# Kernel tuning notes

Measured on AMD Instinct MI355X. Metric: run time of the kernel, lower is better.

## Reference

```python
import jax, jax.numpy as jnp
import numpy as np

N_NODES = 100000
N_EDGES = 1250000
N_PAIRS = 200000
IN_DIM = 128
HID = 64
N_LAYERS = 3


def setup_inputs() -> dict:
    key = jax.random.key(0)
    ks = jax.random.split(key, 16)
    x = jax.random.normal(ks[0], (N_NODES, IN_DIM), dtype=jnp.float32)
    edge_index = jax.random.randint(ks[1], (2, N_EDGES), 0, N_NODES, dtype=jnp.int64)
    pair_index = jax.random.randint(ks[2], (N_PAIRS, 2), 0, N_NODES, dtype=jnp.int64)
    s_in = 1.0 / np.sqrt(IN_DIM)
    s_h = 1.0 / np.sqrt(HID)
    s_2h = 1.0 / np.sqrt(2 * HID)
    enc_W = jax.random.uniform(ks[3], (IN_DIM, HID), jnp.float32, -s_in, s_in)
    enc_b = jax.random.uniform(ks[4], (HID,), jnp.float32, -s_in, s_in)
    # SAGEConv params per layer: lin_l (neighbors, with bias), lin_r (root, no bias)
    Wl = jax.random.uniform(ks[5], (N_LAYERS, HID, HID), jnp.float32, -s_h, s_h)
    bl = jax.random.uniform(ks[6], (N_LAYERS, HID), jnp.float32, -s_h, s_h)
    Wr = jax.random.uniform(ks[7], (N_LAYERS, HID, HID), jnp.float32, -s_h, s_h)
    # predictor MLP: Linear(2h -> h), ReLU, Linear(h -> 1)
    W1 = jax.random.uniform(ks[8], (2 * HID, HID), jnp.float32, -s_2h, s_2h)
    b1 = jax.random.uniform(ks[9], (HID,), jnp.float32, -s_2h, s_2h)
    W2 = jax.random.uniform(ks[10], (HID, 1), jnp.float32, -s_h, s_h)
    b2 = jax.random.uniform(ks[11], (1,), jnp.float32, -s_h, s_h)
    return {"x": x, "edge_index": edge_index, "pair_index": pair_index,
            "enc_W": enc_W, "enc_b": enc_b, "Wl": Wl, "bl": bl, "Wr": Wr,
            "W1": W1, "b1": b1, "W2": W2, "b2": b2}


def reference(x, edge_index, pair_index, enc_W, enc_b, Wl, bl, Wr, W1, b1, W2, b2):
    src, dst = edge_index[0], edge_index[1]
    n = x.shape[0]
    # neighbor counts for mean aggregation (empty neighborhoods -> 0, matching PyG)
    deg = jax.ops.segment_sum(jnp.ones((src.shape[0],), x.dtype), dst, num_segments=n)
    inv_deg = jnp.where(deg > 0, 1.0 / jnp.maximum(deg, 1.0), 0.0)[:, None]  # [N,1]
    # node encoder: Linear + ReLU
    h = jax.nn.relu(x @ enc_W + enc_b)  # [N, HID]
    for i in range(Wl.shape[0]):
        # scatter-mean of source features onto destinations
        agg = jax.ops.segment_sum(h[src], dst, num_segments=n) * inv_deg  # [N, HID]
        h = jax.nn.relu(agg @ Wl[i] + bl[i] + h @ Wr[i])
        # dropout is identity in eval mode
    z = jnp.concatenate([h[pair_index[:, 0]], h[pair_index[:, 1]]], axis=1)  # [P, 2*HID]
    out = (jax.nn.relu(z @ W1 + b1) @ W2 + b2)[:, 0]  # [P]
    return out
```

## Files before the change

### kernel.cpp

```cpp
#include <hip/hip_runtime.h>
#include <hip/hip_fp16.h>
#include <cstdint>
#include <cstddef>

#define N_NODES_C 100000
#define N_EDGES_C 1250000
#define N_PAIRS_C 200000
#define IN_DIM_C 128
#define HID_C 64

#define NB_S 256
#define BSH 9
#define NPB 512
#define NBKT 196
#define SEG_CAP 8192

typedef _Float16 f16x8 __attribute__((ext_vector_type(8)));
typedef float f32x4 __attribute__((ext_vector_type(4)));


#define SCAN_TPB 256
#define SCAN_IPT 4
#define SCAN_ELEMS 1024

__global__ void k_scan_partial(const int* __restrict__ in, int* __restrict__ outp,
                               int* __restrict__ blocksums, int n) {
    __shared__ int sd[SCAN_TPB];
    int tid = threadIdx.x;
    int base = blockIdx.x * SCAN_ELEMS + tid * SCAN_IPT;
    int v[SCAN_IPT]; int s = 0;
    for (int k = 0; k < SCAN_IPT; k++) { int idx = base + k; v[k] = (idx < n) ? in[idx] : 0; s += v[k]; }
    sd[tid] = s;
    __syncthreads();
    for (int off = 1; off < SCAN_TPB; off <<= 1) {
        int t = (tid >= off) ? sd[tid - off] : 0;
        __syncthreads();
        sd[tid] += t;
        __syncthreads();
    }
    int excl = sd[tid] - s;
    for (int k = 0; k < SCAN_IPT; k++) { int idx = base + k; if (idx < n) outp[idx] = excl; excl += v[k]; }
    if (tid == SCAN_TPB - 1) blocksums[blockIdx.x] = sd[tid];
}

__global__ void k_scan_blocks(int* __restrict__ bs, int nb) {
    __shared__ int sd[128];
    int t = threadIdx.x;
    int v = (t < nb) ? bs[t] : 0;
    sd[t] = v;
    __syncthreads();
    for (int off = 1; off < 128; off <<= 1) {
        int u = (t >= off) ? sd[t - off] : 0;
        __syncthreads();
        sd[t] += u;
        __syncthreads();
    }
    if (t < nb) bs[t] = sd[t] - v;
}

__global__ void k_scan_addg(int* __restrict__ arr, const int* __restrict__ bs, int n) {
    int i = blockIdx.x * blockDim.x + threadIdx.x;
    if (i < n) arr[i] += bs[i >> 10];
}


__global__ __launch_bounds__(256) void k_hist(const int* __restrict__ dst,
                                              int* __restrict__ histT, int e) {
    __shared__ int lh[NBKT];
    int tid = threadIdx.x, k = blockIdx.x;
    if (tid < NBKT) lh[tid] = 0;
    __syncthreads();
    int chunk = (e + NB_S - 1) / NB_S;
    int i0 = k * chunk, i1 = min(i0 + chunk, e);
    for (int i = i0 + tid; i < i1; i += 256) atomicAdd(&lh[dst[i] >> BSH], 1);
    __syncthreads();
    if (tid < NBKT) histT[tid * NB_S + k] = lh[tid];
}

__global__ __launch_bounds__(256) void k_scatter(const int* __restrict__ edges,
                                                 const int* __restrict__ offs,
                                                 int2* __restrict__ staging, int e) {
    __shared__ int cur[NBKT];
    int tid = threadIdx.x, k = blockIdx.x;
    if (tid < NBKT) cur[tid] = offs[tid * NB_S + k];
    __syncthreads();
    int chunk = (e + NB_S - 1) / NB_S;
    int i0 = k * chunk, i1 = min(i0 + chunk, e);
    for (int i = i0 + tid; i < i1; i += 256) {
        int s = edges[i];
        int d = edges[e + i];
        int p = atomicAdd(&cur[d >> BSH], 1);
        staging[p] = make_int2(s, d);
    }
}

__global__ __launch_bounds__(256) void k_bucket_fill(const int2* __restrict__ staging,
        const int* __restrict__ offs, int* __restrict__ rowptr,
        float* __restrict__ invd, int* __restrict__ adj, int n, int e) {
    __shared__ int ldeg[NPB];
    __shared__ int lrow[NPB];
    __shared__ int ps[256];
    __shared__ int lseg[SEG_CAP];
    int tid = threadIdx.x, b = blockIdx.x;
    int n0 = b << BSH;
    int nn = min(NPB, n - n0);
    int segBeg = offs[b * NB_S];
    int segEnd = (b == NBKT - 1) ? e : offs[(b + 1) * NB_S];

    ldeg[tid] = 0; ldeg[tid + 256] = 0;
    __syncthreads();
    for (int i = segBeg + tid; i < segEnd; i += 256)
        atomicAdd(&ldeg[staging[i].y - n0], 1);
    __syncthreads();

    int a0 = ldeg[2 * tid], a1 = ldeg[2 * tid + 1];
    int s = a0 + a1;
    ps[tid] = s;
    __syncthreads();
    for (int off = 1; off < 256; off <<= 1) {
        int t = (tid >= off) ? ps[tid - off] : 0;
        __syncthreads();
        ps[tid] += t;
        __syncthreads();
    }
    int excl = ps[tid] - s;
    lrow[2 * tid] = excl;
    lrow[2 * tid + 1] = excl + a0;
    __syncthreads();

    for (int j = tid; j < nn; j += 256) {
        rowptr[n0 + j] = segBeg + lrow[j];
        int d = ldeg[j];
        invd[n0 + j] = (d > 0) ? (1.0f / (float)d) : 0.0f;
    }
    if (b == NBKT - 1 && tid == 0) rowptr[n] = e;
    __syncthreads();

    for (int i = segBeg + tid; i < segEnd; i += 256) {
        int2 ed = staging[i];
        int p = atomicAdd(&lrow[ed.y - n0], 1);
        if (p < SEG_CAP) lseg[p] = ed.x;
        else adj[segBeg + p] = ed.x;
    }
    __syncthreads();

    int m = segEnd - segBeg; if (m > SEG_CAP) m = SEG_CAP;
    for (int p = tid; p < m; p += 256) adj[segBeg + p] = lseg[p];
}


__global__ __launch_bounds__(256) void k_aggregate(const int* __restrict__ rowptr,
        const int* __restrict__ adj, const float* __restrict__ invd,
        const __half* __restrict__ hin16, __half* __restrict__ agg16, int n) {
    int wid = threadIdx.x >> 6, lane = threadIdx.x & 63;
    int nodeA = (blockIdx.x * 4 + wid) * 2;
    if (nodeA >= n) return;
    const int half_ = lane >> 5;
    const int c2 = (lane & 31) * 2;
    int node = nodeA + half_;
    bool valid = node < n;
    int nodec = valid ? node : n - 1;
    int beg = rowptr[nodec], end = rowptr[nodec + 1];
    float accx = 0.f, accy = 0.f;
    for (int e = beg; e < end; e += 8) {
        int idx[8];
        #pragma unroll
        for (int j = 0; j < 8; ++j) {
            int ee = e + j;
            idx[j] = adj[ee < end ? ee : end - 1];
        }
        __half2 v[8];
        #pragma unroll
        for (int j = 0; j < 8; ++j)
            v[j] = *(const __half2*)&hin16[(size_t)idx[j] * HID_C + c2];
        #pragma unroll
        for (int j = 0; j < 8; ++j) {
            float2 f = __half22float2(v[j]);
            bool in = (e + j < end);
            accx += in ? f.x : 0.f;
            accy += in ? f.y : 0.f;
        }
    }
    if (valid) {
        float s = invd[node];
        *(__half2*)&agg16[(size_t)node * HID_C + c2] =
            __floats2half2_rn(accx * s, accy * s);
    }
}


__device__ __forceinline__ float4 ld4(const float* p) { return *(const float4*)p; }


template<int SRC>
__global__ __launch_bounds__(256, 2) void k_mm(
    const float* __restrict__ A1f,
    const __half* __restrict__ A1h, const __half* __restrict__ A2h,
    const float* __restrict__ Ws1, const float* __restrict__ Ws2,
    const float* __restrict__ bias,
    float* __restrict__ outp, __half* __restrict__ out16, int nrows)
{
    __shared__ __half Ah[128 * 128];
    __shared__ __half Bt[64 * 128];
    const int t = threadIdx.x;
    const int g0 = blockIdx.x * 128;

    #pragma unroll
    for (int p = 0; p < 8; ++p) {
        int li = p * 256 + t;
        int r = li >> 4;
        int o = li & 15;
        int g = g0 + r; if (g > nrows - 1) g = nrows - 1;
        f16x8 v;
        if (SRC == 0) {
            const float* src = A1f + (size_t)g * 128 + o * 8;
            float4 f0 = ld4(src), f1 = ld4(src + 4);
            v[0] = (_Float16)f0.x; v[1] = (_Float16)f0.y;
            v[2] = (_Float16)f0.z; v[3] = (_Float16)f0.w;
            v[4] = (_Float16)f1.x; v[5] = (_Float16)f1.y;
            v[6] = (_Float16)f1.z; v[7] = (_Float16)f1.w;
        } else {
            const __half* src = (o < 8) ? (A1h + (size_t)g * 64 + o * 8)
                                        : (A2h + (size_t)g * 64 + (o - 8) * 8);
            v = *(const f16x8*)src;
        }
        *(f16x8*)&Ah[r * 128 + (o ^ (r & 15)) * 8] = v;
    }
    #pragma unroll
    for (int p = 0; p < 32; ++p) {
        int li = p * 256 + t;
        int c = li & 63;
        int k = li >> 6;
        float wv;
        if (SRC == 0) wv = Ws1[k * 64 + c];
        else          wv = (k < 64) ? Ws1[k * 64 + c] : Ws2[(k - 64) * 64 + c];
        Bt[c * 128 + (((k >> 3) ^ (c & 15)) * 8) + (k & 7)] = __float2half(wv);
    }
    __syncthreads();

    const int lane = t & 63;
    const int wid = t >> 6;
    const int R = wid * 32;
    const int lr = lane & 15;
    const int lk = lane >> 4;

    f32x4 acc[2][4];
    #pragma unroll
    for (int fr = 0; fr < 2; ++fr)
        #pragma unroll
        for (int fc = 0; fc < 4; ++fc)
            acc[fr][fc] = (f32x4){0.f, 0.f, 0.f, 0.f};

    #pragma unroll
    for (int ks = 0; ks < 4; ++ks) {
        int o = ks * 4 + lk;
        f16x8 af0, af1;
        {
            int r0 = R + lr;
            int r1 = R + 16 + lr;
            af0 = *(const f16x8*)&Ah[r0 * 128 + (o ^ (r0 & 15)) * 8];
            af1 = *(const f16x8*)&Ah[r1 * 128 + (o ^ (r1 & 15)) * 8];
        }
        #pragma unroll
        for (int fc = 0; fc < 4; ++fc) {
            int c = fc * 16 + lr;
            f16x8 bf = *(const f16x8*)&Bt[c * 128 + (o ^ (c & 15)) * 8];
            acc[0][fc] = __builtin_amdgcn_mfma_f32_16x16x32_f16(af0, bf, acc[0][fc], 0, 0, 0);
            acc[1][fc] = __builtin_amdgcn_mfma_f32_16x16x32_f16(af1, bf, acc[1][fc], 0, 0, 0);
        }
    }

    float bv[4];
    #pragma unroll
    for (int fc = 0; fc < 4; ++fc) bv[fc] = bias[fc * 16 + lr];
    #pragma unroll
    for (int fr = 0; fr < 2; ++fr) {
        #pragma unroll
        for (int j = 0; j < 4; ++j) {
            int gr = g0 + R + fr * 16 + lk * 4 + j;
            if (gr < nrows) {
                #pragma unroll
                for (int fc = 0; fc < 4; ++fc) {
                    int col = fc * 16 + lr;
                    float v = fmaxf(acc[fr][fc][j] + bv[fc], 0.f);
                    outp[(size_t)gr * 64 + col] = v;
                    if (out16) out16[(size_t)gr * 64 + col] = __float2half(v);
                }
            }
        }
    }
}


__global__ __launch_bounds__(256, 2) void k_uvm(
    const float* __restrict__ H, const float* __restrict__ W1,
    float* __restrict__ U, float* __restrict__ V, int nrows)
{
    __shared__ __half Ah[128 * 64];
    __shared__ __half Bt[128 * 64];
    const int t = threadIdx.x;
    const int g0 = blockIdx.x * 128;

    #pragma unroll
    for (int p = 0; p < 4; ++p) {
        int li = p * 256 + t;
        int r = li >> 3;
        int o = li & 7;
        int g = g0 + r; if (g > nrows - 1) g = nrows - 1;
        const float* src = H + (size_t)g * 64 + o * 8;
        float4 f0 = ld4(src), f1 = ld4(src + 4);
        f16x8 v;
        v[0] = (_Float16)f0.x; v[1] = (_Float16)f0.y;
        v[2] = (_Float16)f0.z; v[3] = (_Float16)f0.w;
        v[4] = (_Float16)f1.x; v[5] = (_Float16)f1.y;
        v[6] = (_Float16)f1.z; v[7] = (_Float16)f1.w;
        *(f16x8*)&Ah[r * 64 + (o ^ (r & 7)) * 8] = v;
    }
    #pragma unroll
    for (int p = 0; p < 32; ++p) {
        int li = p * 256 + t;
        int c = li >> 6;
        int k = li & 63;
        float wv = (c < 64) ? W1[k * 64 + c] : W1[(64 + k) * 64 + (c - 64)];
        Bt[c * 64 + (((k >> 3) ^ (c & 7)) * 8) + (k & 7)] = __float2half(wv);
    }
    __syncthreads();

    const int lane = t & 63;
    const int wid = t >> 6;
    const int R = wid * 32;
    const int lr = lane & 15;
    const int lk = lane >> 4;

    f32x4 acc[2][8];
    #pragma unroll
    for (int fr = 0; fr < 2; ++fr)
        #pragma unroll
        for (int fc = 0; fc < 8; ++fc)
            acc[fr][fc] = (f32x4){0.f, 0.f, 0.f, 0.f};

    #pragma unroll
    for (int ks = 0; ks < 2; ++ks) {
        int o = ks * 4 + lk;
        int r0 = R + lr, r1 = R + 16 + lr;
        f16x8 af0 = *(const f16x8*)&Ah[r0 * 64 + (o ^ (r0 & 7)) * 8];
        f16x8 af1 = *(const f16x8*)&Ah[r1 * 64 + (o ^ (r1 & 7)) * 8];
        #pragma unroll
        for (int fc = 0; fc < 8; ++fc) {
            int c = fc * 16 + lr;
            f16x8 bf = *(const f16x8*)&Bt[c * 64 + (o ^ (c & 7)) * 8];
            acc[0][fc] = __builtin_amdgcn_mfma_f32_16x16x32_f16(af0, bf, acc[0][fc], 0, 0, 0);
            acc[1][fc] = __builtin_amdgcn_mfma_f32_16x16x32_f16(af1, bf, acc[1][fc], 0, 0, 0);
        }
    }

    #pragma unroll
    for (int fr = 0; fr < 2; ++fr) {
        #pragma unroll
        for (int j = 0; j < 4; ++j) {
            int gr = g0 + R + fr * 16 + lk * 4 + j;
            if (gr < nrows) {
                #pragma unroll
                for (int fc = 0; fc < 8; ++fc) {
                    int col = fc * 16 + lr;
                    float v = acc[fr][fc][j];
                    if (col < 64) U[(size_t)gr * 64 + col] = v;
                    else          V[(size_t)gr * 64 + (col - 64)] = v;
                }
            }
        }
    }
}

__global__ __launch_bounds__(256) void k_pred(
    const float* __restrict__ U, const float* __restrict__ V,
    const int* __restrict__ pidx, const float* __restrict__ b1,
    const float* __restrict__ W2, const float* __restrict__ b2,
    float* __restrict__ outp, int np)
{
    const int t = threadIdx.x;
    const int lg = t & 15;
    const int p = blockIdx.x * 16 + (t >> 4);
    float4 bv = ld4(b1 + lg * 4);
    float4 wv = ld4(W2 + lg * 4);
    if (p >= np) return;
    int2 ab = ((const int2*)pidx)[p];
    float4 u = ld4(U + (size_t)ab.x * 64 + lg * 4);
    float4 v = ld4(V + (size_t)ab.y * 64 + lg * 4);
    float zx = fmaxf(u.x + v.x + bv.x, 0.f);
    float zy = fmaxf(u.y + v.y + bv.y, 0.f);
    float zz = fmaxf(u.z + v.z + bv.z, 0.f);
    float zw = fmaxf(u.w + v.w + bv.w, 0.f);
    float s = zx * wv.x + zy * wv.y + zz * wv.z + zw * wv.w;
    s += __shfl_down(s, 8, 16);
    s += __shfl_down(s, 4, 16);
    s += __shfl_down(s, 2, 16);
    s += __shfl_down(s, 1, 16);
    if (lg == 0) outp[p] = s + b2[0];
}


extern "C" void kernel_launch(void* const* d_in, const int* in_sizes, int n_in,
                              void* d_out, int out_size, void* d_ws, size_t ws_size,
                              hipStream_t stream) {
    const float* x    = (const float*)d_in[0];
    const int*   edges= (const int*)d_in[1];
    const int*   pair = (const int*)d_in[2];
    const float* encW = (const float*)d_in[3];
    const float* encb = (const float*)d_in[4];
    const float* Wl   = (const float*)d_in[5];
    const float* bl   = (const float*)d_in[6];
    const float* Wr   = (const float*)d_in[7];
    const float* W1   = (const float*)d_in[8];
    const float* b1   = (const float*)d_in[9];
    const float* W2   = (const float*)d_in[10];
    const float* b2   = (const float*)d_in[11];
    float* out = (float*)d_out;

    const int N = N_NODES_C, E = N_EDGES_C, P = N_PAIRS_C;
    const int* dst = edges + E;
    const int M = NBKT * NB_S;

    char* w = (char*)d_ws;
    auto alloc = [&](size_t bytes) { char* p = w; w += (bytes + 255) & ~(size_t)255; return p; };
    int*   rowptr = (int*)alloc((size_t)(N + 1) * 4);
    int*   histT  = (int*)alloc((size_t)M * 4);
    int*   offs   = (int*)alloc((size_t)M * 4);
    int*   bsums  = (int*)alloc(128 * 4);
    float* invd   = (float*)alloc((size_t)N * 4);
    int*   adj    = (int*)alloc((size_t)E * 4);
    float* h0     = (float*)alloc((size_t)N * HID_C * 4);
    float* h1     = (float*)alloc((size_t)N * HID_C * 4);
    float* agg    = (float*)alloc((size_t)N * HID_C * 4);
    __half* h16a  = (__half*)alloc((size_t)N * HID_C * 2);
    __half* h16b  = (__half*)alloc((size_t)N * HID_C * 2);
    __half* agg16 = (__half*)alloc((size_t)N * HID_C * 2);
    int2*  staging= (int2*)agg;

    int nscan = (M + SCAN_ELEMS - 1) / SCAN_ELEMS;

    hipLaunchKernelGGL(k_hist, dim3(NB_S), dim3(256), 0, stream, dst, histT, E);
    hipLaunchKernelGGL(k_scan_partial, dim3(nscan), dim3(SCAN_TPB), 0, stream, histT, offs, bsums, M);
    hipLaunchKernelGGL(k_scan_blocks, dim3(1), dim3(128), 0, stream, bsums, nscan);
    hipLaunchKernelGGL(k_scan_addg, dim3((M + 255) / 256), dim3(256), 0, stream, offs, bsums, M);
    hipLaunchKernelGGL(k_scatter, dim3(NB_S), dim3(256), 0, stream, edges, offs, staging, E);
    hipLaunchKernelGGL(k_bucket_fill, dim3(NBKT), dim3(256), 0, stream, staging, offs, rowptr, invd, adj, N, E);

    const int NB128 = (N + 127) / 128;

    k_mm<0><<<dim3(NB128), dim3(256), 0, stream>>>(
        x, nullptr, nullptr, encW, nullptr, encb, h0, h16a, N);

    float* hc = h0; float* hn = h1;
    __half* h16c = h16a; __half* h16n = h16b;
    for (int l = 0; l < 3; l++) {
        hipLaunchKernelGGL(k_aggregate, dim3((N / 2 + 3) / 4), dim3(256), 0, stream,
                           rowptr, adj, invd, h16c, agg16, N);
        k_mm<1><<<dim3(NB128), dim3(256), 0, stream>>>(
            nullptr, agg16, h16c, Wl + (size_t)l * 64 * 64, Wr + (size_t)l * 64 * 64,
            bl + (size_t)l * 64, hn, (l < 2) ? h16n : (__half*)nullptr, N);
        float* tswap = hc; hc = hn; hn = tswap;
        __half* t16 = h16c; h16c = h16n; h16n = t16;
    }

    float* Ubuf = agg;
    float* Vbuf = hn;
    const int NB_UV = (N + 127) / 128;
    hipLaunchKernelGGL(k_uvm, dim3(NB_UV), dim3(256), 0, stream, hc, W1, Ubuf, Vbuf, N);
    hipLaunchKernelGGL(k_pred, dim3((P + 15) / 16), dim3(256), 0, stream,
                       Ubuf, Vbuf, pair, b1, W2, b2, out, P);
}
```

Before: 341.5 us.

## Widen aggregation to 4 nodes per wave and store U/V in fp16

The aggregate kernel now has each wave handle four nodes with 16 lanes per node, and each lane loads 8 bytes (four fp16 values) per neighbour instead of 4 bytes. The predictor intermediates U and V are written and gathered as fp16 instead of fp32, which halves the random-gather traffic in the pair predictor. The W1 staging loop is reindexed so consecutive threads read consecutive global columns. The cost is extra fp16 rounding in U and V, plus per-lane indirection overhead that is now spread across fewer lanes.

```diff
diff --git a/kernel.cpp b/kernel.cpp
--- a/kernel.cpp
+++ b/kernel.cpp
@@ -153,15 +153,15 @@
         const int* __restrict__ adj, const float* __restrict__ invd,
         const __half* __restrict__ hin16, __half* __restrict__ agg16, int n) {
     int wid = threadIdx.x >> 6, lane = threadIdx.x & 63;
-    int nodeA = (blockIdx.x * 4 + wid) * 2;
-    if (nodeA >= n) return;
-    const int half_ = lane >> 5;
-    const int c2 = (lane & 31) * 2;
-    int node = nodeA + half_;
+    int node0 = (blockIdx.x * 4 + wid) * 4;
+    if (node0 >= n) return;
+    const int q = lane >> 4;
+    const int c4 = (lane & 15) * 4;
+    int node = node0 + q;
     bool valid = node < n;
     int nodec = valid ? node : n - 1;
     int beg = rowptr[nodec], end = rowptr[nodec + 1];
-    float accx = 0.f, accy = 0.f;
+    float a0 = 0.f, a1 = 0.f, a2 = 0.f, a3 = 0.f;
     for (int e = beg; e < end; e += 8) {
         int idx[8];
         #pragma unroll
@@ -169,22 +169,29 @@
             int ee = e + j;
             idx[j] = adj[ee < end ? ee : end - 1];
         }
-        __half2 v[8];
+        float2 raw[8];
         #pragma unroll
         for (int j = 0; j < 8; ++j)
-            v[j] = *(const __half2*)&hin16[(size_t)idx[j] * HID_C + c2];
+            raw[j] = *(const float2*)&hin16[(size_t)idx[j] * HID_C + c4];
         #pragma unroll
         for (int j = 0; j < 8; ++j) {
-            float2 f = __half22float2(v[j]);
+            union { float f; __half2 h; } ulo, uhi;
+            ulo.f = raw[j].x; uhi.f = raw[j].y;
+            float2 f0 = __half22float2(ulo.h);
+            float2 f1 = __half22float2(uhi.h);
             bool in = (e + j < end);
-            accx += in ? f.x : 0.f;
-            accy += in ? f.y : 0.f;
+            a0 += in ? f0.x : 0.f;
+            a1 += in ? f0.y : 0.f;
+            a2 += in ? f1.x : 0.f;
+            a3 += in ? f1.y : 0.f;
         }
     }
     if (valid) {
         float s = invd[node];
-        *(__half2*)&agg16[(size_t)node * HID_C + c2] =
-            __floats2half2_rn(accx * s, accy * s);
+        union { float f; __half2 h; } s0, s1;
+        s0.h = __floats2half2_rn(a0 * s, a1 * s);
+        s1.h = __floats2half2_rn(a2 * s, a3 * s);
+        *(float2*)&agg16[(size_t)node * HID_C + c4] = make_float2(s0.f, s1.f);
     }
 }
 
@@ -294,7 +301,7 @@
 
 __global__ __launch_bounds__(256, 2) void k_uvm(
     const float* __restrict__ H, const float* __restrict__ W1,
-    float* __restrict__ U, float* __restrict__ V, int nrows)
+    __half* __restrict__ U16, __half* __restrict__ V16, int nrows)
 {
     __shared__ __half Ah[128 * 64];
     __shared__ __half Bt[128 * 64];
@@ -319,8 +326,8 @@
     #pragma unroll
     for (int p = 0; p < 32; ++p) {
         int li = p * 256 + t;
-        int c = li >> 6;
-        int k = li & 63;
+        int c = li & 127;
+        int k = li >> 7;
         float wv = (c < 64) ? W1[k * 64 + c] : W1[(64 + k) * 64 + (c - 64)];
         Bt[c * 64 + (((k >> 3) ^ (c & 7)) * 8) + (k & 7)] = __float2half(wv);
     }
@@ -363,9 +370,9 @@
                 #pragma unroll
                 for (int fc = 0; fc < 8; ++fc) {
                     int col = fc * 16 + lr;
-                    float v = acc[fr][fc][j];
-                    if (col < 64) U[(size_t)gr * 64 + col] = v;
-                    else          V[(size_t)gr * 64 + (col - 64)] = v;
+                    __half v = __float2half(acc[fr][fc][j]);
+                    if (col < 64) U16[(size_t)gr * 64 + col] = v;
+                    else          V16[(size_t)gr * 64 + (col - 64)] = v;
                 }
             }
         }
@@ -373,7 +380,7 @@
 }
 
 __global__ __launch_bounds__(256) void k_pred(
-    const float* __restrict__ U, const float* __restrict__ V,
+    const __half* __restrict__ U16, const __half* __restrict__ V16,
     const int* __restrict__ pidx, const float* __restrict__ b1,
     const float* __restrict__ W2, const float* __restrict__ b2,
     float* __restrict__ outp, int np)
@@ -385,12 +392,16 @@
     float4 wv = ld4(W2 + lg * 4);
     if (p >= np) return;
     int2 ab = ((const int2*)pidx)[p];
-    float4 u = ld4(U + (size_t)ab.x * 64 + lg * 4);
-    float4 v = ld4(V + (size_t)ab.y * 64 + lg * 4);
-    float zx = fmaxf(u.x + v.x + bv.x, 0.f);
-    float zy = fmaxf(u.y + v.y + bv.y, 0.f);
-    float zz = fmaxf(u.z + v.z + bv.z, 0.f);
-    float zw = fmaxf(u.w + v.w + bv.w, 0.f);
+    float2 ur = *(const float2*)&U16[(size_t)ab.x * 64 + lg * 4];
+    float2 vr = *(const float2*)&V16[(size_t)ab.y * 64 + lg * 4];
+    union { float f; __half2 h; } u0, u1, v0, v1;
+    u0.f = ur.x; u1.f = ur.y; v0.f = vr.x; v1.f = vr.y;
+    float2 ua = __half22float2(u0.h), ub = __half22float2(u1.h);
+    float2 va = __half22float2(v0.h), vb = __half22float2(v1.h);
+    float zx = fmaxf(ua.x + va.x + bv.x, 0.f);
+    float zy = fmaxf(ua.y + va.y + bv.y, 0.f);
+    float zz = fmaxf(ub.x + vb.x + bv.z, 0.f);
+    float zw = fmaxf(ub.y + vb.y + bv.w, 0.f);
     float s = zx * wv.x + zy * wv.y + zz * wv.z + zw * wv.w;
     s += __shfl_down(s, 8, 16);
     s += __shfl_down(s, 4, 16);
@@ -435,6 +446,8 @@
     __half* h16a  = (__half*)alloc((size_t)N * HID_C * 2);
     __half* h16b  = (__half*)alloc((size_t)N * HID_C * 2);
     __half* agg16 = (__half*)alloc((size_t)N * HID_C * 2);
+    __half* U16   = (__half*)alloc((size_t)N * HID_C * 2);
+    __half* V16   = (__half*)alloc((size_t)N * HID_C * 2);
     int2*  staging= (int2*)agg;
 
     int nscan = (M + SCAN_ELEMS - 1) / SCAN_ELEMS;
@@ -454,7 +467,7 @@
     float* hc = h0; float* hn = h1;
     __half* h16c = h16a; __half* h16n = h16b;
     for (int l = 0; l < 3; l++) {
-        hipLaunchKernelGGL(k_aggregate, dim3((N / 2 + 3) / 4), dim3(256), 0, stream,
+        hipLaunchKernelGGL(k_aggregate, dim3((N + 15) / 16), dim3(256), 0, stream,
                            rowptr, adj, invd, h16c, agg16, N);
         k_mm<1><<<dim3(NB128), dim3(256), 0, stream>>>(
             nullptr, agg16, h16c, Wl + (size_t)l * 64 * 64, Wr + (size_t)l * 64 * 64,
@@ -463,10 +476,8 @@
         __half* t16 = h16c; h16c = h16n; h16n = t16;
     }
 
-    float* Ubuf = agg;
-    float* Vbuf = hn;
     const int NB_UV = (N + 127) / 128;
-    hipLaunchKernelGGL(k_uvm, dim3(NB_UV), dim3(256), 0, stream, hc, W1, Ubuf, Vbuf, N);
+    hipLaunchKernelGGL(k_uvm, dim3(NB_UV), dim3(256), 0, stream, hc, W1, U16, V16, N);
     hipLaunchKernelGGL(k_pred, dim3((P + 15) / 16), dim3(256), 0, stream,
-                       Ubuf, Vbuf, pair, b1, W2, b2, out, P);
-}
+                       U16, V16, pair, b1, W2, b2, out, P);
+}
```

After: 329.8 us. 3.5% less time.
